# Kernel tuning notes

Measured on AMD Instinct MI355X. Metric: run time of the kernel, lower is better.

Reference implementation:

```python
import jax, jax.numpy as jnp
import numpy as np
from jax import lax

B, INP, OUP, H, W = 16, 128, 128, 56, 56
EXPAND = 6
HID = INP * EXPAND  # 768
EPS = 1e-5


def setup_inputs() -> dict:
    key = jax.random.key(0)
    ks = jax.random.split(key, 18)
    x = jax.random.normal(ks[0], (B, INP, H, W), dtype=jnp.float32)
    mask = jax.random.randint(ks[1], (B, 1, H, W), 0, 2, dtype=jnp.int32)
    w1 = jax.random.normal(ks[2], (HID, INP), dtype=jnp.float32) * 0.05
    g1 = 1.0 + 0.1 * jax.random.normal(ks[3], (HID,), dtype=jnp.float32)
    b1 = 0.1 * jax.random.normal(ks[4], (HID,), dtype=jnp.float32)
    m1 = 0.1 * jax.random.normal(ks[5], (HID,), dtype=jnp.float32)
    v1 = jax.random.uniform(ks[6], (HID,), dtype=jnp.float32) + 0.5
    wdw = jax.random.normal(ks[7], (HID, 1, 3, 3), dtype=jnp.float32) * 0.05
    g2 = 1.0 + 0.1 * jax.random.normal(ks[8], (HID,), dtype=jnp.float32)
    b2 = 0.1 * jax.random.normal(ks[9], (HID,), dtype=jnp.float32)
    m2 = 0.1 * jax.random.normal(ks[10], (HID,), dtype=jnp.float32)
    v2 = jax.random.uniform(ks[11], (HID,), dtype=jnp.float32) + 0.5
    w2 = jax.random.normal(ks[12], (OUP, HID), dtype=jnp.float32) * 0.05
    g3 = 1.0 + 0.1 * jax.random.normal(ks[13], (OUP,), dtype=jnp.float32)
    b3 = 0.1 * jax.random.normal(ks[14], (OUP,), dtype=jnp.float32)
    m3 = 0.1 * jax.random.normal(ks[15], (OUP,), dtype=jnp.float32)
    v3 = jax.random.uniform(ks[16], (OUP,), dtype=jnp.float32) + 0.5
    return dict(x=x, w1=w1, g1=g1, b1=b1, m1=m1, v1=v1, wdw=wdw,
                g2=g2, b2=b2, m2=m2, v2=v2, w2=w2,
                g3=g3, b3=b3, m3=m3, v3=v3, mask=mask)


def _bn(h, g, b, m, v):
    # inference-mode BatchNorm2d: (h - mean) * gamma/sqrt(var+eps) + beta
    scale = g / jnp.sqrt(v + EPS)
    return (h - m[None, :, None, None]) * scale[None, :, None, None] + b[None, :, None, None]


def reference(x, w1, g1, b1, m1, v1, wdw, g2, b2, m2, v2, w2, g3, b3, m3, v3, mask):
    mf = mask.astype(x.dtype)  # [B,1,H,W] binary mask ('std')
    # mask_dilate: 3x3 binary dilation (dilate_stride=1) so the depthwise conv
    # has valid neighbors for every active output pixel
    md = lax.reduce_window(mf, 0.0, lax.max, (1, 1, 3, 3), (1, 1, 1, 1), 'SAME')
    # expand 1x1 conv + BN + ReLU6, restricted to dilated mask
    h = jnp.einsum('bchw,kc->bkhw', x, w1)            # [B,HID,H,W]
    h = jnp.clip(_bn(h, g1, b1, m1, v1), 0.0, 6.0) * md
    # depthwise 3x3 conv + BN + ReLU6, restricted to std mask
    h = lax.conv_general_dilated(h, wdw, (1, 1), 'SAME',
                                 feature_group_count=HID,
                                 dimension_numbers=('NCHW', 'OIHW', 'NCHW'))
    h = jnp.clip(_bn(h, g2, b2, m2, v2), 0.0, 6.0) * mf
    # project 1x1 conv + BN (no relu), restricted to std mask
    h = jnp.einsum('bkhw,ok->bohw', h, w2)            # [B,OUP,H,W]
    h = _bn(h, g3, b3, m3, v3) * mf
    # scatter-add into identity path
    return x + h
```

## Files before the change

kernel.cpp:

```cpp
#include <hip/hip_runtime.h>
#include <hip/hip_bf16.h>

#define BATCH 16
#define INP   128
#define OUP   128
#define HH    56
#define WW    56
#define HWSZ  3136
#define HID   768
#define EPSV  1e-5f

#define PXST  33
#define RWST2 1920
#define H2STR 66
#define XSTR  130

typedef __attribute__((ext_vector_type(8))) short bf16x8;
typedef __attribute__((ext_vector_type(4))) float f32x4;
typedef __attribute__((ext_vector_type(2))) float f32x2;

__device__ __forceinline__ unsigned short f2b(float f) {
    unsigned u = __float_as_uint(f);
    return (unsigned short)((u + 0x7FFFu + ((u >> 16) & 1u)) >> 16);
}
__device__ __forceinline__ float blo(unsigned u){ return __uint_as_float(u << 16); }
__device__ __forceinline__ float bhi(unsigned u){ return __uint_as_float(u & 0xFFFF0000u); }
__device__ __forceinline__ unsigned pkbf(float lo, float hi) {
    unsigned r;
    asm("v_cvt_pk_bf16_f32 %0, %1, %2" : "=v"(r) : "v"(lo), "v"(hi));
    return r;
}
__device__ __forceinline__ void pkfma(f32x2& a, f32x2 b, f32x2 c) {
    asm("v_pk_fma_f32 %0, %1, %2, %0" : "+v"(a) : "v"(b), "v"(c));
}

__global__ void prep(const float* __restrict__ w1, const float* __restrict__ g1,
                     const float* __restrict__ b1, const float* __restrict__ m1, const float* __restrict__ v1,
                     const float* __restrict__ wdw, const float* __restrict__ g2,
                     const float* __restrict__ b2, const float* __restrict__ m2, const float* __restrict__ v2,
                     const float* __restrict__ w2, const float* __restrict__ g3,
                     const float* __restrict__ b3, const float* __restrict__ m3, const float* __restrict__ v3,
                     const int* __restrict__ mask,
                     unsigned short* __restrict__ w1f, unsigned short* __restrict__ w2f,
                     float* __restrict__ be1o, float* __restrict__ wdsf,
                     float* __restrict__ be2o, float* __restrict__ be3o,
                     float* __restrict__ mdf, float* __restrict__ mff)
{
    int gid = blockIdx.x * blockDim.x + threadIdx.x;
    int stp = gridDim.x * blockDim.x;
    for (int i = gid; i < HID * INP; i += stp) {
        int r = i >> 7, k = i & 127;
        float s = g1[r] * rsqrtf(v1[r] + EPSV);
        int ht = r >> 4, r16 = r & 15, ks = k >> 5, g = (k >> 3) & 3, e = k & 7;
        w1f[((((ht * 4 + ks) * 4 + g) * 16 + r16) << 3) + e] = f2b(w1[i] * s);
    }
    for (int i = gid; i < OUP * HID; i += stp) {
        int r = i / HID, k = i - r * HID;
        float s = g3[r] * rsqrtf(v3[r] + EPSV);
        int ot = r >> 4, r16 = r & 15, ch = k >> 6, ks = (k >> 5) & 1, g = (k >> 3) & 3, e = k & 7;
        int lane = g * 16 + r16;
        w2f[((((ot * 12 + ch) * 2 + ks) * 64 + lane) << 3) + e] = f2b(w2[i] * s);
    }
    for (int i = gid; i < HID; i += stp) {
        float s1 = g1[i] * rsqrtf(v1[i] + EPSV);
        be1o[i] = b1[i] - m1[i] * s1;
        float s2 = g2[i] * rsqrtf(v2[i] + EPSV);
        be2o[i] = b2[i] - m2[i] * s2;
    }
    for (int i = gid; i < HID * 9; i += stp) {
        int q = i / HID, c = i - q * HID;
        float s2 = g2[c] * rsqrtf(v2[c] + EPSV);
        wdsf[i] = wdw[c * 9 + q] * s2;
    }
    for (int i = gid; i < OUP; i += stp) {
        float s3 = g3[i] * rsqrtf(v3[i] + EPSV);
        be3o[i] = b3[i] - m3[i] * s3;
    }
    for (int i = gid; i < BATCH * HWSZ; i += stp) {
        int b = i / HWSZ, p = i - b * HWSZ;
        int y = p / WW, xx = p - y * WW;
        float mf = (float)mask[i];
        float md = 0.f;
        for (int dy = -1; dy <= 1; ++dy)
            for (int dx = -1; dx <= 1; ++dx) {
                int yy = y + dy, xc = xx + dx;
                if (yy >= 0 && yy < HH && xc >= 0 && xc < WW)
                    md = fmaxf(md, (float)mask[b * HWSZ + yy * WW + xc]);
            }
        mff[i] = mf;
        mdf[i] = md;
    }
}

__launch_bounds__(512, 4)
__global__ void k1_expand(const float* __restrict__ x,
                          const unsigned short* __restrict__ w1f,
                          const float* __restrict__ be1g,
                          const float* __restrict__ mdf,
                          unsigned* __restrict__ h1p)
{
    __shared__ unsigned short xs[128 * XSTR];
    const int t = threadIdx.x, lane = t & 63, wv = t >> 6;
    const int g = lane >> 4, r16 = lane & 15;
    const int pid = blockIdx.x;
    const int l = (pid & 7) * 150 + (pid >> 3);
    const int hb = l % 3;
    const int pb = (l / 3) % 25;
    const int b  = l / 75;
    const int p0 = pb * 128;
    const int whid = wv & 3;
    const int wpx  = wv >> 2;

    for (int rep = 0; rep < 8; ++rep) {
        int id = t + rep * 512;
        int px = id & 127, c4 = id >> 7;
        int p = p0 + px;
        ushort4 u; u.x = 0; u.y = 0; u.z = 0; u.w = 0;
        if (p < HWSZ) {
            const float* xp = x + ((size_t)(b * INP + c4 * 4)) * HWSZ + p;
            unsigned lo = pkbf(xp[0], xp[HWSZ]);
            unsigned hi = pkbf(xp[2 * HWSZ], xp[3 * HWSZ]);
            u.x = (unsigned short)lo; u.y = (unsigned short)(lo >> 16);
            u.z = (unsigned short)hi; u.w = (unsigned short)(hi >> 16);
        }
        *(ushort4*)&xs[px * XSTR + (((c4 >> 1) ^ (px & 15)) << 3) + ((c4 & 1) << 2)] = u;
    }
    __syncthreads();

    f32x4 acc[4][4];
    #pragma unroll
    for (int mt = 0; mt < 4; ++mt)
        #pragma unroll
        for (int nt = 0; nt < 4; ++nt) {
            acc[mt][nt][0] = 0.f; acc[mt][nt][1] = 0.f;
            acc[mt][nt][2] = 0.f; acc[mt][nt][3] = 0.f;
        }
    const int hbase = hb * 256 + whid * 64;
    const int htb = hbase >> 4;

    #pragma unroll
    for (int ks = 0; ks < 4; ++ks) {
        bf16x8 af[4];
        #pragma unroll
        for (int mt = 0; mt < 4; ++mt)
            af[mt] = *(const bf16x8*)&w1f[((((htb + mt) * 4 + ks) * 64) + lane) << 3];
        #pragma unroll
        for (int nt = 0; nt < 4; ++nt) {
            int px = wpx * 64 + nt * 16 + r16;
            bf16x8 bf = *(const bf16x8*)&xs[px * XSTR + (((ks * 4 + g) ^ r16) << 3)];
            #pragma unroll
            for (int mt = 0; mt < 4; ++mt)
                acc[mt][nt] = __builtin_amdgcn_mfma_f32_16x16x32_bf16(af[mt], bf, acc[mt][nt], 0, 0, 0);
        }
    }

    #pragma unroll
    for (int nt = 0; nt < 4; ++nt) {
        const int pg = p0 + wpx * 64 + nt * 16;
        if (pg >= HWSZ) continue;
        const int p = pg + r16;
        const float md = mdf[b * HWSZ + p];
        #pragma unroll
        for (int mt = 0; mt < 4; ++mt) {
            const float4 be4 = *(const float4*)&be1g[hbase + mt * 16 + g * 4];
            f32x4 a = acc[mt][nt];
            float v0 = fminf(fmaxf(a[0] + be4.x, 0.f), 6.f) * md;
            float v1 = fminf(fmaxf(a[1] + be4.y, 0.f), 6.f) * md;
            float v2 = fminf(fmaxf(a[2] + be4.z, 0.f), 6.f) * md;
            float v3 = fminf(fmaxf(a[3] + be4.w, 0.f), 6.f) * md;
            const int c2 = (hbase >> 1) + mt * 8 + g * 2;
            const size_t ad = (size_t)(b * 384 + c2) * HWSZ + p;
            h1p[ad] = pkbf(v0, v1);
            h1p[ad + HWSZ] = pkbf(v2, v3);
        }
    }
}

__launch_bounds__(512, 4)
__global__ void k23(const unsigned* __restrict__ h1p,
                    const unsigned short* __restrict__ w2f,
                    const float* __restrict__ wdsf,
                    const float* __restrict__ be2g,
                    const float* __restrict__ be3g,
                    const float* __restrict__ mff,
                    const float* __restrict__ x,
                    float* __restrict__ out)
{
    __shared__ unsigned stg[4 * RWST2];
    __shared__ unsigned short h2s[112 * H2STR];
    __shared__ float mfv_[112];

    const int t = threadIdx.x, lane = t & 63, wv = t >> 6;
    const int g = lane >> 4, r16 = lane & 15;
    const int pid = blockIdx.x;
    const int l = (pid & 7) * 56 + (pid >> 3);
    const int strip = l % 28, b = l / 28;
    const int y0 = strip * 2, p0 = strip * 112;

    if (t < 112) mfv_[t] = mff[b * HWSZ + p0 + t];
    if (t >= 128 && t < 384) {
        int i = t - 128;
        int cp = i & 31, row = (i >> 5) & 3, side = (i >> 7) & 1;
        stg[row * RWST2 + (side ? 57 * PXST : 0) + cp] = 0;
    }

    int gaddr[7], laddr[7]; bool gval[7];
    #pragma unroll
    for (int rep = 0; rep < 7; ++rep) {
        const int id = t + rep * 512;
        const int rr = (id * 2341) >> 16;
        const int p2 = id - rr * 28;
        const int cp = rr >> 2, row = rr & 3;
        const int gy = y0 - 1 + row;
        gval[rep] = gy >= 0 && gy < HH;
        gaddr[rep] = (b * 384 + cp) * HWSZ + gy * WW + 2 * p2;
        laddr[rep] = row * RWST2 + (2 * p2 + 1) * PXST + cp;
    }
    uint2 sreg[7];

    auto issueLoads = [&]() {
        #pragma unroll
        for (int rep = 0; rep < 7; ++rep) {
            uint2 u; u.x = 0; u.y = 0;
            if (gval[rep]) u = *(const uint2*)&h1p[gaddr[rep]];
            sreg[rep] = u;
            gaddr[rep] += 32 * HWSZ;
        }
    };
    auto stageWrite = [&]() {
        #pragma unroll
        for (int rep = 0; rep < 7; ++rep) {
            stg[laddr[rep]] = sreg[rep].x;
            stg[laddr[rep] + PXST] = sreg[rep].y;
        }
    };

    const int cp_c = t & 31, row2 = (t >> 5) & 1, q = t >> 6;
    unsigned* const h2d = (unsigned*)h2s;

    auto phaseDW = [&](int ch) {
        f32x2 acc2[7];
        {
            const float2 be2 = *(const float2*)&be2g[ch * 64 + 2 * cp_c];
            #pragma unroll
            for (int j = 0; j < 7; ++j) { acc2[j][0] = be2.x; acc2[j][1] = be2.y; }
        }
        #pragma unroll
        for (int dy = 0; dy < 3; ++dy) {
            f32x2 wt0 = *(const f32x2*)&wdsf[(dy * 3 + 0) * HID + ch * 64 + 2 * cp_c];
            f32x2 wt1 = *(const f32x2*)&wdsf[(dy * 3 + 1) * HID + ch * 64 + 2 * cp_c];
            f32x2 wt2 = *(const f32x2*)&wdsf[(dy * 3 + 2) * HID + ch * 64 + 2 * cp_c];
            const unsigned* rp = &stg[(row2 + dy) * RWST2 + (q * 7) * PXST + cp_c];
            f32x2 p[9];
            #pragma unroll
            for (int k = 0; k < 9; ++k) {
                unsigned u = rp[k * PXST];
                p[k][0] = blo(u); p[k][1] = bhi(u);
            }
            #pragma unroll
            for (int j = 0; j < 7; ++j) {
                pkfma(acc2[j], p[j], wt0);
                pkfma(acc2[j], p[j + 1], wt1);
                pkfma(acc2[j], p[j + 2], wt2);
            }
        }
        #pragma unroll
        for (int j = 0; j < 7; ++j) {
            const int px = row2 * 56 + q * 7 + j;
            const float mv = mfv_[px];
            float vL = __builtin_amdgcn_fmed3f(acc2[j][0], 0.f, 6.f) * mv;
            float vH = __builtin_amdgcn_fmed3f(acc2[j][1], 0.f, 6.f) * mv;
            h2d[px * 33 + cp_c] = pkbf(vL, vH);
        }
    };

    f32x4 pacc[7];
    #pragma unroll
    for (int nt = 0; nt < 7; ++nt) {
        pacc[nt][0] = 0.f; pacc[nt][1] = 0.f; pacc[nt][2] = 0.f; pacc[nt][3] = 0.f;
    }

    auto phaseP = [&](int ch) {
        #pragma unroll
        for (int ks = 0; ks < 2; ++ks) {
            const bf16x8 pw = *(const bf16x8*)&w2f[((((wv * 12 + ch) * 2 + ks) * 64) + lane) << 3];
            #pragma unroll
            for (int nt = 0; nt < 7; ++nt) {
                const int px = nt * 16 + r16;
                const bf16x8 hb = *(const bf16x8*)&h2s[px * H2STR + (ks * 4 + g) * 8];
                pacc[nt] = __builtin_amdgcn_mfma_f32_16x16x32_bf16(pw, hb, pacc[nt], 0, 0, 0);
            }
        }
    };

    issueLoads();
    stageWrite();
    __syncthreads();
    for (int ch = 0; ch < 12; ++ch) {
        if (ch + 1 < 12) issueLoads();
        phaseDW(ch);
        __syncthreads();
        if (ch + 1 < 12) stageWrite();
        phaseP(ch);
        __syncthreads();
    }

    {
        const int ob = wv * 16 + g * 4;
        const float4 be4 = *(const float4*)&be3g[ob];
        #pragma unroll
        for (int nt = 0; nt < 7; ++nt) {
            const int px = nt * 16 + r16;
            const float mv = mfv_[px];
            const size_t base = (size_t)(b * OUP + ob) * HWSZ + p0 + px;
            out[base]            = x[base]            + (pacc[nt][0] + be4.x) * mv;
            out[base + HWSZ]     = x[base + HWSZ]     + (pacc[nt][1] + be4.y) * mv;
            out[base + 2 * HWSZ] = x[base + 2 * HWSZ] + (pacc[nt][2] + be4.z) * mv;
            out[base + 3 * HWSZ] = x[base + 3 * HWSZ] + (pacc[nt][3] + be4.w) * mv;
        }
    }
}

extern "C" void kernel_launch(void* const* d_in, const int* in_sizes, int n_in,
                              void* d_out, int out_size, void* d_ws, size_t ws_size,
                              hipStream_t stream) {
    (void)in_sizes; (void)n_in; (void)out_size; (void)ws_size;
    const float* x   = (const float*)d_in[0];
    const float* w1  = (const float*)d_in[1];
    const float* g1  = (const float*)d_in[2];
    const float* b1  = (const float*)d_in[3];
    const float* m1  = (const float*)d_in[4];
    const float* v1  = (const float*)d_in[5];
    const float* wdw = (const float*)d_in[6];
    const float* g2  = (const float*)d_in[7];
    const float* b2  = (const float*)d_in[8];
    const float* m2  = (const float*)d_in[9];
    const float* v2  = (const float*)d_in[10];
    const float* w2  = (const float*)d_in[11];
    const float* g3  = (const float*)d_in[12];
    const float* b3  = (const float*)d_in[13];
    const float* m3  = (const float*)d_in[14];
    const float* v3  = (const float*)d_in[15];
    const int*  mask = (const int*)d_in[16];
    float* out = (float*)d_out;

    char* ws = (char*)d_ws;
    unsigned short* w1f = (unsigned short*)ws;
    unsigned short* w2f = (unsigned short*)(ws + 196608);
    float* be1o = (float*)(ws + 393216);
    float* wdsf = (float*)(ws + 396288);
    float* be2o = (float*)(ws + 423936);
    float* be3o = (float*)(ws + 427008);
    float* mdf  = (float*)(ws + 427520);
    float* mff  = (float*)(ws + 628224);
    unsigned* h1p = (unsigned*)(ws + 828928);

    prep<<<256, 256, 0, stream>>>(w1, g1, b1, m1, v1, wdw, g2, b2, m2, v2,
                                  w2, g3, b3, m3, v3, mask,
                                  w1f, w2f, be1o, wdsf, be2o, be3o, mdf, mff);
    k1_expand<<<dim3(1200), 512, 0, stream>>>(x, w1f, be1o, mdf, h1p);
    k23<<<dim3(448), 512, 0, stream>>>(h1p, w2f, wdsf, be2o, be3o, mff, x, out);
}
```

Baseline: 101.7 us.

## Pad h1 layout with halo rows and stage via direct global-to-LDS loads

```diff
diff --git a/kernel.cpp b/kernel.cpp
--- a/kernel.cpp
+++ b/kernel.cpp
@@ -10,14 +10,17 @@
 #define HID   768
 #define EPSV  1e-5f
 
-#define PXST  33
-#define RWST2 1920
-#define H2STR 66
+#define CPST  265
+#define H2STR 72
 #define XSTR  130
+#define H1ROW 64
+#define H1RPC 58
 
 typedef __attribute__((ext_vector_type(8))) short bf16x8;
 typedef __attribute__((ext_vector_type(4))) float f32x4;
 typedef __attribute__((ext_vector_type(2))) float f32x2;
+typedef __attribute__((address_space(1))) const unsigned GU;
+typedef __attribute__((address_space(3))) unsigned LU;
 
 __device__ __forceinline__ unsigned short f2b(float f) {
     unsigned u = __float_as_uint(f);
@@ -44,7 +47,8 @@
                      unsigned short* __restrict__ w1f, unsigned short* __restrict__ w2f,
                      float* __restrict__ be1o, float* __restrict__ wdsf,
                      float* __restrict__ be2o, float* __restrict__ be3o,
-                     float* __restrict__ mdf, float* __restrict__ mff)
+                     float* __restrict__ mdf, float* __restrict__ mff,
+                     unsigned* __restrict__ h1p)
 {
     int gid = blockIdx.x * blockDim.x + threadIdx.x;
     int stp = gridDim.x * blockDim.x;
@@ -89,6 +93,15 @@
             }
         mff[i] = mf;
         mdf[i] = md;
+    }
+    for (int i = gid; i < BATCH * 384 * 2 * H1ROW; i += stp) {
+        int rr = i >> 6, d = i & 63;
+        int bcp = rr >> 1, side = rr & 1;
+        h1p[((size_t)bcp * H1RPC + (side ? 57 : 0)) * H1ROW + d] = 0;
+    }
+    for (int i = gid; i < BATCH * 384 * 56 * 8; i += stp) {
+        int rr = i >> 3, d = i & 7;
+        h1p[((size_t)(rr / 56) * H1RPC + 1 + (rr % 56)) * H1ROW + (d < 4 ? d : 56 + d)] = 0;
     }
 }
 
@@ -159,6 +172,8 @@
         const int pg = p0 + wpx * 64 + nt * 16;
         if (pg >= HWSZ) continue;
         const int p = pg + r16;
+        const int row = (p * 9363) >> 19;
+        const int col = p - row * 56;
         const float md = mdf[b * HWSZ + p];
         #pragma unroll
         for (int mt = 0; mt < 4; ++mt) {
@@ -169,9 +184,9 @@
             float v2 = fminf(fmaxf(a[2] + be4.z, 0.f), 6.f) * md;
             float v3 = fminf(fmaxf(a[3] + be4.w, 0.f), 6.f) * md;
             const int c2 = (hbase >> 1) + mt * 8 + g * 2;
-            const size_t ad = (size_t)(b * 384 + c2) * HWSZ + p;
+            const size_t ad = ((size_t)(b * 384 + c2) * H1RPC + row + 1) * H1ROW + 4 + col;
             h1p[ad] = pkbf(v0, v1);
-            h1p[ad + HWSZ] = pkbf(v2, v3);
+            h1p[ad + H1RPC * H1ROW] = pkbf(v2, v3);
         }
     }
 }
@@ -186,7 +201,7 @@
                     const float* __restrict__ x,
                     float* __restrict__ out)
 {
-    __shared__ unsigned stg[4 * RWST2];
+    __shared__ unsigned stg[32 * CPST];
     __shared__ unsigned short h2s[112 * H2STR];
     __shared__ float mfv_[112];
 
@@ -198,41 +213,20 @@
     const int y0 = strip * 2, p0 = strip * 112;
 
     if (t < 112) mfv_[t] = mff[b * HWSZ + p0 + t];
-    if (t >= 128 && t < 384) {
-        int i = t - 128;
-        int cp = i & 31, row = (i >> 5) & 3, side = (i >> 7) & 1;
-        stg[row * RWST2 + (side ? 57 * PXST : 0) + cp] = 0;
-    }
-
-    int gaddr[7], laddr[7]; bool gval[7];
-    #pragma unroll
-    for (int rep = 0; rep < 7; ++rep) {
-        const int id = t + rep * 512;
-        const int rr = (id * 2341) >> 16;
-        const int p2 = id - rr * 28;
-        const int cp = rr >> 2, row = rr & 3;
-        const int gy = y0 - 1 + row;
-        gval[rep] = gy >= 0 && gy < HH;
-        gaddr[rep] = (b * 384 + cp) * HWSZ + gy * WW + 2 * p2;
-        laddr[rep] = row * RWST2 + (2 * p2 + 1) * PXST + cp;
-    }
-    uint2 sreg[7];
-
-    auto issueLoads = [&]() {
-        #pragma unroll
-        for (int rep = 0; rep < 7; ++rep) {
-            uint2 u; u.x = 0; u.y = 0;
-            if (gval[rep]) u = *(const uint2*)&h1p[gaddr[rep]];
-            sreg[rep] = u;
-            gaddr[rep] += 32 * HWSZ;
-        }
-    };
-    auto stageWrite = [&]() {
-        #pragma unroll
-        for (int rep = 0; rep < 7; ++rep) {
-            stg[laddr[rep]] = sreg[rep].x;
-            stg[laddr[rep] + PXST] = sreg[rep].y;
-        }
+
+    const unsigned* gb[4];
+    unsigned* lb[4];
+    #pragma unroll
+    for (int i = 0; i < 4; ++i) {
+        const int cpw = wv * 4 + i;
+        gb[i] = h1p + (((size_t)(b * 384 + cpw) * H1RPC + y0) << 6) + lane * 4;
+        lb[i] = &stg[cpw * CPST];
+    }
+    auto dma = [&](int ch) {
+        #pragma unroll
+        for (int i = 0; i < 4; ++i)
+            __builtin_amdgcn_global_load_lds((GU*)(gb[i] + (size_t)ch * 32 * H1RPC * H1ROW),
+                                             (LU*)lb[i], 16, 0, 0);
     };
 
     const int cp_c = t & 31, row2 = (t >> 5) & 1, q = t >> 6;
@@ -245,16 +239,17 @@
             #pragma unroll
             for (int j = 0; j < 7; ++j) { acc2[j][0] = be2.x; acc2[j][1] = be2.y; }
         }
+        const int w0d = q * 7 + 3;
         #pragma unroll
         for (int dy = 0; dy < 3; ++dy) {
             f32x2 wt0 = *(const f32x2*)&wdsf[(dy * 3 + 0) * HID + ch * 64 + 2 * cp_c];
             f32x2 wt1 = *(const f32x2*)&wdsf[(dy * 3 + 1) * HID + ch * 64 + 2 * cp_c];
             f32x2 wt2 = *(const f32x2*)&wdsf[(dy * 3 + 2) * HID + ch * 64 + 2 * cp_c];
-            const unsigned* rp = &stg[(row2 + dy) * RWST2 + (q * 7) * PXST + cp_c];
+            const unsigned* rb = &stg[cp_c * CPST + (row2 + dy) * H1ROW + w0d];
             f32x2 p[9];
             #pragma unroll
             for (int k = 0; k < 9; ++k) {
-                unsigned u = rp[k * PXST];
+                unsigned u = rb[k];
                 p[k][0] = blo(u); p[k][1] = bhi(u);
             }
             #pragma unroll
@@ -270,53 +265,52 @@
             const float mv = mfv_[px];
             float vL = __builtin_amdgcn_fmed3f(acc2[j][0], 0.f, 6.f) * mv;
             float vH = __builtin_amdgcn_fmed3f(acc2[j][1], 0.f, 6.f) * mv;
-            h2d[px * 33 + cp_c] = pkbf(vL, vH);
+            h2d[px * 36 + (((cp_c >> 2) ^ (px & 7)) << 2) + (cp_c & 3)] = pkbf(vL, vH);
         }
     };
 
-    f32x4 pacc[7];
-    #pragma unroll
-    for (int nt = 0; nt < 7; ++nt) {
-        pacc[nt][0] = 0.f; pacc[nt][1] = 0.f; pacc[nt][2] = 0.f; pacc[nt][3] = 0.f;
-    }
+    f32x4 pacc[8];
+    #pragma unroll
+    for (int ot = 0; ot < 8; ++ot) {
+        pacc[ot][0] = 0.f; pacc[ot][1] = 0.f; pacc[ot][2] = 0.f; pacc[ot][3] = 0.f;
+    }
+    const int ppx = wv * 16 + r16;
 
     auto phaseP = [&](int ch) {
-        #pragma unroll
-        for (int ks = 0; ks < 2; ++ks) {
-            const bf16x8 pw = *(const bf16x8*)&w2f[((((wv * 12 + ch) * 2 + ks) * 64) + lane) << 3];
-            #pragma unroll
-            for (int nt = 0; nt < 7; ++nt) {
-                const int px = nt * 16 + r16;
-                const bf16x8 hb = *(const bf16x8*)&h2s[px * H2STR + (ks * 4 + g) * 8];
-                pacc[nt] = __builtin_amdgcn_mfma_f32_16x16x32_bf16(pw, hb, pacc[nt], 0, 0, 0);
+        if (wv < 7) {
+            #pragma unroll
+            for (int ks = 0; ks < 2; ++ks) {
+                const bf16x8 hb = *(const bf16x8*)&h2s[ppx * H2STR + (((ks * 4 + g) ^ (ppx & 7)) << 3)];
+                #pragma unroll
+                for (int ot = 0; ot < 8; ++ot) {
+                    const bf16x8 pw = *(const bf16x8*)&w2f[((((ot * 12 + ch) * 2 + ks) * 64) + lane) << 3];
+                    pacc[ot] = __builtin_amdgcn_mfma_f32_16x16x32_bf16(pw, hb, pacc[ot], 0, 0, 0);
+                }
             }
         }
     };
 
-    issueLoads();
-    stageWrite();
+    dma(0);
     __syncthreads();
     for (int ch = 0; ch < 12; ++ch) {
-        if (ch + 1 < 12) issueLoads();
         phaseDW(ch);
         __syncthreads();
-        if (ch + 1 < 12) stageWrite();
+        if (ch + 1 < 12) dma(ch + 1);
         phaseP(ch);
         __syncthreads();
     }
 
-    {
-        const int ob = wv * 16 + g * 4;
-        const float4 be4 = *(const float4*)&be3g[ob];
-        #pragma unroll
-        for (int nt = 0; nt < 7; ++nt) {
-            const int px = nt * 16 + r16;
-            const float mv = mfv_[px];
-            const size_t base = (size_t)(b * OUP + ob) * HWSZ + p0 + px;
-            out[base]            = x[base]            + (pacc[nt][0] + be4.x) * mv;
-            out[base + HWSZ]     = x[base + HWSZ]     + (pacc[nt][1] + be4.y) * mv;
-            out[base + 2 * HWSZ] = x[base + 2 * HWSZ] + (pacc[nt][2] + be4.z) * mv;
-            out[base + 3 * HWSZ] = x[base + 3 * HWSZ] + (pacc[nt][3] + be4.w) * mv;
+    if (wv < 7) {
+        const float mv = mfv_[ppx];
+        #pragma unroll
+        for (int ot = 0; ot < 8; ++ot) {
+            const int ob = ot * 16 + g * 4;
+            const float4 be4 = *(const float4*)&be3g[ob];
+            const size_t base = (size_t)(b * OUP + ob) * HWSZ + p0 + ppx;
+            out[base]            = x[base]            + (pacc[ot][0] + be4.x) * mv;
+            out[base + HWSZ]     = x[base + HWSZ]     + (pacc[ot][1] + be4.y) * mv;
+            out[base + 2 * HWSZ] = x[base + 2 * HWSZ] + (pacc[ot][2] + be4.z) * mv;
+            out[base + 3 * HWSZ] = x[base + 3 * HWSZ] + (pacc[ot][3] + be4.w) * mv;
         }
     }
 }
@@ -357,7 +351,7 @@
 
     prep<<<256, 256, 0, stream>>>(w1, g1, b1, m1, v1, wdw, g2, b2, m2, v2,
                                   w2, g3, b3, m3, v3, mask,
-                                  w1f, w2f, be1o, wdsf, be2o, be3o, mdf, mff);
+                                  w1f, w2f, be1o, wdsf, be2o, be3o, mdf, mff, h1p);
     k1_expand<<<dim3(1200), 512, 0, stream>>>(x, w1f, be1o, mdf, h1p);
     k23<<<dim3(448), 512, 0, stream>>>(h1p, w2f, wdsf, be2o, be3o, mff, x, out);
 }
```

Result: slower. 105.1 us (+3.3%).
